# Optimization experiments

Measured on AMD Instinct MI355X. Metric: run time of the kernel, lower is better.

Reference implementation:

```python
import jax, jax.numpy as jnp
import numpy as np

V, D, B, L, A = 50000, 512, 64, 512, 4


def setup_inputs() -> dict:
    key = jax.random.key(0)
    ks = jax.random.split(key, 9)
    emb = jax.random.normal(ks[0], (V, D), jnp.float32) * 0.02
    emb = emb.at[0].set(0.0)  # padding_idx=0 row is zero
    s = 1.0 / np.sqrt(D)
    W_ih = jax.random.uniform(ks[1], (4 * D, 2 * D), jnp.float32, -s, s)
    W_hh = jax.random.uniform(ks[2], (4 * D, D), jnp.float32, -s, s)
    b_ih = jax.random.uniform(ks[3], (4 * D,), jnp.float32, -s, s)
    b_hh = jax.random.uniform(ks[4], (4 * D,), jnp.float32, -s, s)
    X = jax.random.randint(ks[5], (B, L), 0, V, dtype=jnp.int32)
    X_lengths = jax.random.randint(ks[6], (B,), 1, L + 1, dtype=jnp.int32)
    aspect = jax.random.randint(ks[7], (B, A), 0, V, dtype=jnp.int32)
    aspect_lengths = jax.random.randint(ks[8], (B,), 1, A + 1, dtype=jnp.int32)
    return dict(X=X, X_lengths=X_lengths, aspect=aspect, aspect_lengths=aspect_lengths,
                emb=emb, W_ih=W_ih, W_hh=W_hh, b_ih=b_ih, b_hh=b_hh)


def _lstm(embedded, mask, W_ih, W_hh, b_ih, b_hh):
    # embedded: [B, L, 2D], mask: [B, L] bool. Emulates packed LSTM: state only
    # advances on valid steps; padded outputs are zero (pad_packed_sequence).
    Bn = embedded.shape[0]
    Dh = W_hh.shape[1]
    # Precompute input projection for all steps: [L, B, 4D]
    x_proj = (jnp.einsum('blg,hg->blh', embedded, W_ih) + b_ih + b_hh).transpose(1, 0, 2)
    m_seq = mask.T  # [L, B]
    h0 = jnp.zeros((Bn, Dh), embedded.dtype)

    def step(carry, inp):
        h, c = carry
        x_t, m_t = inp
        gates = x_t + h @ W_hh.T  # [B, 4D]
        i, f, g, o = jnp.split(gates, 4, axis=-1)  # PyTorch gate order i,f,g,o
        i = jax.nn.sigmoid(i)
        f = jax.nn.sigmoid(f)
        g = jnp.tanh(g)
        o = jax.nn.sigmoid(o)
        c_new = f * c + i * g
        h_new = o * jnp.tanh(c_new)
        m = m_t[:, None]
        h = jnp.where(m, h_new, h)
        c = jnp.where(m, c_new, c)
        out = jnp.where(m, h_new, jnp.zeros_like(h_new))
        return (h, c), out

    (hT, _), outs = jax.lax.scan(step, (h0, h0), (x_proj, m_seq))
    return outs.transpose(1, 0, 2), hT  # [B, L, D], [B, D]


def reference(X, X_lengths, aspect, aspect_lengths, emb, W_ih, W_hh, b_ih, b_hh):
    word_emb = emb[X]  # [B, L, D]
    # Original uses self.embedding for the aspect ids too (faithful to source).
    asp_emb = emb[aspect].sum(axis=1) / aspect_lengths[:, None].astype(emb.dtype)  # [B, D]
    mask = jnp.arange(word_emb.shape[1])[None, :] < X_lengths[:, None]  # [B, L]
    embedded = jnp.concatenate(
        [word_emb, jnp.broadcast_to(asp_emb[:, None, :], word_emb.shape)], axis=-1)
    embedded = embedded * mask[:, :, None]  # positions >= length stay zero
    output, hT = _lstm(embedded, mask, W_ih, W_hh, b_ih, b_hh)
    hidden = hT[None]  # [1, B, D] like torch (num_layers, B, D)
    return output, hidden, asp_emb
```

## Files before the change

kernel.cpp:

```cpp
#include <hip/hip_runtime.h>


using f32x4  = __attribute__((ext_vector_type(4))) float;
using s16x4  = __attribute__((ext_vector_type(4))) short;
using bf16x8 = __attribute__((ext_vector_type(8))) __bf16;

#define LOG2E 1.4426950408889634f

__device__ __forceinline__ float b2f(short s) {
  union { unsigned u; float f; } c;
  c.u = ((unsigned)(unsigned short)s) << 16;
  return c.f;
}
__device__ __forceinline__ short f2bf(float f) {
  union { float f; unsigned u; } c; c.f = f;
  unsigned r = (c.u + 0x7FFFu + ((c.u >> 16) & 1u)) >> 16;
  return (short)(unsigned short)r;
}
__device__ __forceinline__ float sigm_(float x) {
  float e = __builtin_amdgcn_exp2f(-x * LOG2E);
  return __builtin_amdgcn_rcpf(1.0f + e);
}
__device__ __forceinline__ float tanh_(float x) {
  float e = __builtin_amdgcn_exp2f(x * (2.0f * LOG2E));
  return 1.0f - 2.0f * __builtin_amdgcn_rcpf(1.0f + e);
}

__global__ void k_asp(const int* __restrict__ aspect, const int* __restrict__ alen,
                      const float* __restrict__ emb, float* __restrict__ asp_emb,
                      float* __restrict__ out_asp, unsigned* __restrict__ hbuf) {
  int b = blockIdx.x;
  int t = threadIdx.x;
  {
    unsigned* hz = hbuf + (size_t)(b * 128 + t) * 8;
    #pragma unroll
    for (int i = 0; i < 8; ++i) hz[i] = 0u;
  }
  f32x4 s = {0.f, 0.f, 0.f, 0.f};
  #pragma unroll
  for (int a = 0; a < 4; ++a) {
    int idx = aspect[b * 4 + a];
    s += *(const f32x4*)(emb + (size_t)idx * 512 + t * 4);
  }
  float inv = 1.0f / (float)alen[b];
  s[0] *= inv; s[1] *= inv; s[2] *= inv; s[3] *= inv;
  *(f32x4*)(asp_emb + (size_t)b * 512 + t * 4) = s;
  *(f32x4*)(out_asp + (size_t)b * 512 + t * 4) = s;
}

__global__ void k_pack(const float* __restrict__ W_ih, const float* __restrict__ W_hh,
                       short* __restrict__ W1p, short* __restrict__ Whp) {
  int P = blockIdx.x;
  int t = threadIdx.x;
  int gr = (P & 3) * 512 + (P >> 5) * 8 + ((P >> 2) & 7);
  f32x4 w1 = *(const f32x4*)(W_ih + (size_t)gr * 1024 + t * 4);
  s16x4 o1, oh;
  #pragma unroll
  for (int i = 0; i < 4; ++i) {
    o1[i] = f2bf(w1[i]);
    int c = t * 4 + i;
    int ks = (c & ~7) | (((c & 1) << 2) | ((c >> 1) & 3));
    oh[i] = f2bf(W_hh[(size_t)gr * 512 + ks]);
  }
  *(s16x4*)(W1p + (size_t)P * 512 + t * 4) = o1;
  *(s16x4*)(Whp + (size_t)P * 512 + t * 4) = oh;
}

__global__ void k_aspc(const float* __restrict__ asp_emb, const float* __restrict__ W_ih,
                       const float* __restrict__ b_ih, const float* __restrict__ b_hh,
                       float* __restrict__ aspc) {
  int tid = threadIdx.x;
  int P = blockIdx.x * 32 + (tid >> 3);
  int gr = (P & 3) * 512 + (P >> 5) * 8 + ((P >> 2) & 7);
  const float* wrow = W_ih + (size_t)gr * 1024 + 512;
  float bias = b_ih[gr] + b_hh[gr];
  int b0 = (tid & 7) * 8;
  float a[8];
  #pragma unroll
  for (int i = 0; i < 8; ++i) a[i] = 0.f;
  for (int k = 0; k < 512; k += 4) {
    f32x4 wv = *(const f32x4*)(wrow + k);
    #pragma unroll
    for (int bb = 0; bb < 8; ++bb) {
      f32x4 av = *(const f32x4*)(asp_emb + (size_t)(b0 + bb) * 512 + k);
      a[bb] += wv[0] * av[0] + wv[1] * av[1] + wv[2] * av[2] + wv[3] * av[3];
    }
  }
  #pragma unroll
  for (int bb = 0; bb < 8; ++bb) aspc[(size_t)(b0 + bb) * 2048 + P] = a[bb] + bias;
}

__global__ void k_gather(const int* __restrict__ X, const int* __restrict__ xlen,
                         const float* __restrict__ emb, short* __restrict__ word) {
  int g = blockIdx.x * 256 + threadIdx.x;
  int row = g >> 7;
  int k4 = (g & 127) << 2;
  int b = row >> 9, l = row & 511;
  s16x4 o;
  if (l < xlen[b]) {
    int idx = X[row];
    f32x4 v = *(const f32x4*)(emb + (size_t)idx * 512 + k4);
    o[0] = f2bf(v[0]); o[1] = f2bf(v[1]); o[2] = f2bf(v[2]); o[3] = f2bf(v[3]);
  } else {
    o[0] = 0; o[1] = 0; o[2] = 0; o[3] = 0;
  }
  *(s16x4*)(word + (size_t)row * 512 + k4) = o;
}

__global__ __launch_bounds__(256)
void k_gemm(const short* __restrict__ A, const short* __restrict__ B,
            const float* __restrict__ aspc, const int* __restrict__ xlen,
            short* __restrict__ C) {
  __shared__ char smem[65536];
  const int rt = blockIdx.x, ct = blockIdx.y;
  const int b = rt >> 2;
  if (xlen[b] <= ((rt & 3) << 7)) return;
  const int tid = threadIdx.x;
  const int w = tid >> 6, lane = tid & 63;
  const int lr = lane & 15, lg = lane >> 4;
  const int wr = (w & 1) * 64, wc = (w >> 1) * 64;
  const char* Ab = (const char*)(A + (size_t)rt * 128 * 512);
  const char* Bb = (const char*)(B + (size_t)ct * 128 * 512);

  f32x4 acc[4][4];
  #pragma unroll
  for (int mi = 0; mi < 4; ++mi)
    #pragma unroll
    for (int ni = 0; ni < 4; ++ni) acc[mi][ni] = {0.f, 0.f, 0.f, 0.f};

  auto stage = [&](int kt, int buf) {
    #pragma unroll
    for (int p = 0; p < 4; ++p) {
      int dbase = w * 1024 + p * 4096;
      int d = dbase + (lane << 4);
      int row = d >> 7;
      int kb = (d & 127) ^ (((d >> 9) & 1) << 5);
      __builtin_amdgcn_global_load_lds(
          (const __attribute__((address_space(1))) unsigned*)(Ab + (size_t)row * 1024 + kt * 128 + kb),
          (__attribute__((address_space(3))) unsigned*)(smem + buf * 16384 + dbase), 16, 0, 0);
      __builtin_amdgcn_global_load_lds(
          (const __attribute__((address_space(1))) unsigned*)(Bb + (size_t)row * 1024 + kt * 128 + kb),
          (__attribute__((address_space(3))) unsigned*)(smem + 32768 + buf * 16384 + dbase), 16, 0, 0);
    }
  };

  stage(0, 0);
  __syncthreads();
  #pragma unroll 1
  for (int kt = 0; kt < 8; ++kt) {
    int cur = kt & 1;
    if (kt < 7) stage(kt + 1, cur ^ 1);
    const char* sAc = smem + cur * 16384;
    const char* sBc = smem + 32768 + cur * 16384;
    #pragma unroll
    for (int kk = 0; kk < 2; ++kk) {
      bf16x8 af[4], bfr[4];
      #pragma unroll
      for (int mi = 0; mi < 4; ++mi) {
        int lin = (wr + mi * 16 + lr) * 128 + kk * 64 + lg * 16;
        af[mi] = *(const bf16x8*)(sAc + (lin ^ (((lin >> 9) & 1) << 5)));
      }
      #pragma unroll
      for (int ni = 0; ni < 4; ++ni) {
        int lin = (wc + ni * 16 + lr) * 128 + kk * 64 + lg * 16;
        bfr[ni] = *(const bf16x8*)(sBc + (lin ^ (((lin >> 9) & 1) << 5)));
      }
      #pragma unroll
      for (int mi = 0; mi < 4; ++mi)
        #pragma unroll
        for (int ni = 0; ni < 4; ++ni)
          acc[mi][ni] = __builtin_amdgcn_mfma_f32_16x16x32_bf16(af[mi], bfr[ni], acc[mi][ni], 0, 0, 0);
    }
    __syncthreads();
  }

  const int colb = ct * 128 + wc;
  float cb[4];
  #pragma unroll
  for (int ni = 0; ni < 4; ++ni) cb[ni] = aspc[(size_t)b * 2048 + colb + ni * 16 + lr];
  #pragma unroll
  for (int mi = 0; mi < 4; ++mi) {
    const int row0 = rt * 128 + wr + mi * 16 + lg * 4;
    #pragma unroll
    for (int r = 0; r < 4; ++r) {
      short* crow = C + (size_t)(row0 + r) * 2048 + colb + lr;
      #pragma unroll
      for (int ni = 0; ni < 4; ++ni)
        crow[ni * 16] = f2bf(acc[mi][ni][r] + cb[ni]);
    }
  }
}

__global__ __launch_bounds__(256, 1)
void k_rnn(const short* __restrict__ xproj, const short* __restrict__ Whp,
           const int* __restrict__ xlen, unsigned* hbuf, float* __restrict__ out) {
  __shared__ char wlds[32768];
  const int j = blockIdx.x;
  const int tid = threadIdx.x;
  const int w = tid >> 6;
  const int lane = tid & 63;
  const int lr = lane & 15, lg = lane >> 4;
  const int batch = w * 16 + lr;
  const int mylen = xlen[batch];

  int nt = xlen[batch];
  #pragma unroll
  for (int d = 8; d; d >>= 1) nt = max(nt, __shfl_xor(nt, d));

  {
    const char* src = (const char*)(Whp + (size_t)j * 32 * 512);
    int base = tid * 128;
    int row = base >> 10;
    int c0 = base & 1023;
    #pragma unroll
    for (int i = 0; i < 8; ++i) {
      int c = c0 + i * 16;
      *(f32x4*)(wlds + row * 1024 + (c ^ ((row & 7) << 4))) =
          *(const f32x4*)(src + (size_t)row * 1024 + c);
    }
  }
  __syncthreads();

  float cc0 = 0.f, cc1 = 0.f, h0 = 0.f, h1 = 0.f;
  const short* xbase = xproj + (size_t)batch * 512 * 2048 + j * 32 + lg * 4;
  float* outb = out + (size_t)batch * 512 * 512 + (size_t)j * 8 + lg;
  char* hbB = (char*)hbuf;

  s16x4 xc0 = *(const s16x4*)(xbase);
  s16x4 xc1 = *(const s16x4*)(xbase + 16);
  int i1 = (1 < nt) ? 1 : 0;
  s16x4 xn0 = *(const s16x4*)(xbase + (size_t)i1 * 2048);
  s16x4 xn1 = *(const s16x4*)(xbase + (size_t)i1 * 2048 + 16);

  #pragma unroll 1
  for (int t = 0; t < nt; ++t) {
    f32x4 acc0 = {0.f, 0.f, 0.f, 0.f}, acc1 = {0.f, 0.f, 0.f, 0.f};
    if (t > 0) {
      const char* hb = hbB + (size_t)((t - 1) & 1) * 131072 + batch * 32;
      const unsigned tneed = (unsigned)t;
      int4 qa[16], qb[16];
      unsigned pend = 0xffffu;
      while (pend) {
        #pragma unroll
        for (int kk = 0; kk < 16; ++kk)
          if (pend & (1u << kk)) {
            const char* p = hb + (size_t)(kk * 4 + lg) * 2048;
            asm volatile("global_load_dwordx4 %0, %1, off sc0 sc1"
                         : "=&v"(qa[kk]) : "v"(p) : "memory");
            asm volatile("global_load_dwordx4 %0, %1, off sc0 sc1"
                         : "=&v"(qb[kk]) : "v"(p + 16) : "memory");
          }
        asm volatile("s_waitcnt vmcnt(0)" ::: "memory");
        __builtin_amdgcn_sched_barrier(0);
        #pragma unroll
        for (int kk = 0; kk < 16; ++kk)
          if (pend & (1u << kk)) {
            int4 q0 = qa[kk], q1 = qb[kk];
            unsigned m0 = min((unsigned)q0.x & 0xffffu, (unsigned)q0.y & 0xffffu);
            unsigned m1 = min((unsigned)q0.z & 0xffffu, (unsigned)q0.w & 0xffffu);
            unsigned m2 = min((unsigned)q1.x & 0xffffu, (unsigned)q1.y & 0xffffu);
            unsigned m3 = min((unsigned)q1.z & 0xffffu, (unsigned)q1.w & 0xffffu);
            unsigned mn = min(min(m0, m1), min(m2, m3));
            if (__all(mn >= tneed)) pend &= ~(1u << kk);
          }
      }
      __builtin_amdgcn_sched_barrier(0);
      #pragma unroll
      for (int kk = 0; kk < 16; ++kk) {
        int4 q0 = qa[kk], q1 = qb[kk];
        union { unsigned u[4]; bf16x8 v; } pk;
        pk.u[0] = ((unsigned)q0.x >> 16) | ((unsigned)q0.y & 0xffff0000u);
        pk.u[1] = ((unsigned)q0.z >> 16) | ((unsigned)q0.w & 0xffff0000u);
        pk.u[2] = ((unsigned)q1.x >> 16) | ((unsigned)q1.y & 0xffff0000u);
        pk.u[3] = ((unsigned)q1.z >> 16) | ((unsigned)q1.w & 0xffff0000u);
        int sw = (kk * 64 + lg * 16) ^ ((lr & 7) << 4);
        bf16x8 a0 = *(const bf16x8*)(wlds + lr * 1024 + sw);
        bf16x8 a1 = *(const bf16x8*)(wlds + (16 + lr) * 1024 + sw);
        acc0 = __builtin_amdgcn_mfma_f32_16x16x32_bf16(a0, pk.v, acc0, 0, 0, 0);
        acc1 = __builtin_amdgcn_mfma_f32_16x16x32_bf16(a1, pk.v, acc1, 0, 0, 0);
      }
    }

    const bool m = (t < mylen);
    float hn0, hn1;
    {
      float gi = acc0[0] + b2f(xc0[0]);
      float gf = acc0[1] + b2f(xc0[1]);
      float gg = acc0[2] + b2f(xc0[2]);
      float go = acc0[3] + b2f(xc0[3]);
      float ii = sigm_(gi), ff = sigm_(gf), gv = tanh_(gg), oo = sigm_(go);
      float cn = ff * cc0 + ii * gv;
      hn0 = oo * tanh_(cn);
      cc0 = m ? cn : cc0;
      h0 = m ? hn0 : h0;
    }
    {
      float gi = acc1[0] + b2f(xc1[0]);
      float gf = acc1[1] + b2f(xc1[1]);
      float gg = acc1[2] + b2f(xc1[2]);
      float go = acc1[3] + b2f(xc1[3]);
      float ii = sigm_(gi), ff = sigm_(gf), gv = tanh_(gg), oo = sigm_(go);
      float cn = ff * cc1 + ii * gv;
      hn1 = oo * tanh_(cn);
      cc1 = m ? cn : cc1;
      h1 = m ? hn1 : h1;
    }

    {
      unsigned tag = (unsigned)(t + 1) & 0xffffu;
      unsigned d0 = ((unsigned)(unsigned short)f2bf(h0) << 16) | tag;
      unsigned d1 = ((unsigned)(unsigned short)f2bf(h1) << 16) | tag;
      unsigned long long pr = (unsigned long long)d0 | ((unsigned long long)d1 << 32);
      char* hw = hbB + (size_t)(t & 1) * 131072 + j * 2048 + batch * 32 + lg * 8;
      asm volatile("global_store_dwordx2 %0, %1, off sc0 sc1"
                   :: "v"(hw), "v"(pr) : "memory");
    }

    outb[(size_t)t * 512] = m ? hn0 : 0.0f;
    outb[(size_t)t * 512 + 4] = m ? hn1 : 0.0f;
    int tn = (t + 2 < nt) ? t + 2 : nt - 1;
    const short* xp = xbase + (size_t)tn * 2048;
    xc0 = xn0; xc1 = xn1;
    xn0 = *(const s16x4*)(xp);
    xn1 = *(const s16x4*)(xp + 16);
  }

  for (int t = nt; t < 512; ++t) {
    outb[(size_t)t * 512] = 0.0f;
    outb[(size_t)t * 512 + 4] = 0.0f;
  }

  float* oh = out + (size_t)64 * 512 * 512 + (size_t)batch * 512 + j * 8;
  oh[lg] = h0;
  oh[4 + lg] = h1;
}

extern "C" void kernel_launch(void* const* d_in, const int* in_sizes, int n_in,
                              void* d_out, int out_size, void* d_ws, size_t ws_size,
                              hipStream_t stream) {
  const int*   X      = (const int*)d_in[0];
  const int*   Xlen   = (const int*)d_in[1];
  const int*   aspect = (const int*)d_in[2];
  const int*   alen   = (const int*)d_in[3];
  const float* emb    = (const float*)d_in[4];
  const float* W_ih   = (const float*)d_in[5];
  const float* W_hh   = (const float*)d_in[6];
  const float* b_ih   = (const float*)d_in[7];
  const float* b_hh   = (const float*)d_in[8];
  float* out = (float*)d_out;

  char* ws = (char*)d_ws;
  float*    asp_emb = (float*)(ws + 0);
  float*    aspc    = (float*)(ws + 131072);
  short*    W1p     = (short*)(ws + 655360);
  short*    Whp     = (short*)(ws + 2752512);
  unsigned* hbuf    = (unsigned*)(ws + 4849664);
  short*    word    = (short*)(ws + 5111808);
  short*    xproj   = (short*)(ws + 38666240);

  float* out_hT  = out + (size_t)64 * 512 * 512;
  float* out_asp = out_hT + (size_t)64 * 512;

  hipLaunchKernelGGL(k_asp,    dim3(64),        dim3(128), 0, stream,
                     aspect, alen, emb, asp_emb, out_asp, hbuf);
  hipLaunchKernelGGL(k_pack,   dim3(2048),      dim3(128), 0, stream,
                     W_ih, W_hh, W1p, Whp);
  hipLaunchKernelGGL(k_aspc,   dim3(64),        dim3(256), 0, stream,
                     asp_emb, W_ih, b_ih, b_hh, aspc);
  hipLaunchKernelGGL(k_gather, dim3(16384),     dim3(256), 0, stream,
                     X, Xlen, emb, word);
  hipLaunchKernelGGL(k_gemm,   dim3(256, 16),   dim3(256), 0, stream,
                     word, W1p, aspc, Xlen, xproj);
  hipLaunchKernelGGL(k_rnn,    dim3(64),        dim3(256), 0, stream,
                     xproj, Whp, Xlen, hbuf, out);
}
```

Baseline: 2.100 ms.

## Split LSTM recurrence across 256 blocks grouped per XCC with local/global handoff

The recurrent kernel moves from 64 blocks, each owning hidden units for all batches, to 256 blocks. Each block claims a role through an atomic counter so that the 32 blocks on one XCC share one group of 8 batches. Hidden states are published twice, to a buffer read with XCC-local coherence (sc0) and to a globally coherent copy. Readers poll the local copy first and fall back to the global one, with the aim of cutting cross-die latency in the per-step barrier. The packed W_hh layout and the gate-row permutation change to match, and the risk is role claims failing to land on the expected XCC or stale reads from the non-coherent path.

New measurement: 7.424 ms. 3.54x slower.

```diff
diff --git a/kernel.cpp b/kernel.cpp
--- a/kernel.cpp
+++ b/kernel.cpp
@@ -25,17 +25,23 @@
   float e = __builtin_amdgcn_exp2f(x * (2.0f * LOG2E));
   return 1.0f - 2.0f * __builtin_amdgcn_rcpf(1.0f + e);
 }
+__device__ __forceinline__ void vmcnt0() {
+  asm volatile("s_waitcnt vmcnt(0)" ::: "memory");
+}
 
 __global__ void k_asp(const int* __restrict__ aspect, const int* __restrict__ alen,
                       const float* __restrict__ emb, float* __restrict__ asp_emb,
-                      float* __restrict__ out_asp, unsigned* __restrict__ hbuf) {
+                      float* __restrict__ out_asp, char* __restrict__ zero_mb,
+                      int* __restrict__ role_claim) {
   int b = blockIdx.x;
   int t = threadIdx.x;
   {
-    unsigned* hz = hbuf + (size_t)(b * 128 + t) * 8;
-    #pragma unroll
-    for (int i = 0; i < 8; ++i) hz[i] = 0u;
-  }
+    f32x4 z = {0.f, 0.f, 0.f, 0.f};
+    char* p = zero_mb + (size_t)(b * 128 + t) * 64;
+    *(f32x4*)(p) = z; *(f32x4*)(p + 16) = z;
+    *(f32x4*)(p + 32) = z; *(f32x4*)(p + 48) = z;
+  }
+  if (b >= 62) role_claim[(b - 62) * 128 + t] = 0;
   f32x4 s = {0.f, 0.f, 0.f, 0.f};
   #pragma unroll
   for (int a = 0; a < 4; ++a) {
@@ -52,16 +58,12 @@
                        short* __restrict__ W1p, short* __restrict__ Whp) {
   int P = blockIdx.x;
   int t = threadIdx.x;
-  int gr = (P & 3) * 512 + (P >> 5) * 8 + ((P >> 2) & 7);
+  int gr = (P & 3) * 512 + (P >> 6) * 16 + ((P >> 2) & 15);
   f32x4 w1 = *(const f32x4*)(W_ih + (size_t)gr * 1024 + t * 4);
+  f32x4 wh = *(const f32x4*)(W_hh + (size_t)gr * 512 + t * 4);
   s16x4 o1, oh;
   #pragma unroll
-  for (int i = 0; i < 4; ++i) {
-    o1[i] = f2bf(w1[i]);
-    int c = t * 4 + i;
-    int ks = (c & ~7) | (((c & 1) << 2) | ((c >> 1) & 3));
-    oh[i] = f2bf(W_hh[(size_t)gr * 512 + ks]);
-  }
+  for (int i = 0; i < 4; ++i) { o1[i] = f2bf(w1[i]); oh[i] = f2bf(wh[i]); }
   *(s16x4*)(W1p + (size_t)P * 512 + t * 4) = o1;
   *(s16x4*)(Whp + (size_t)P * 512 + t * 4) = oh;
 }
@@ -71,7 +73,7 @@
                        float* __restrict__ aspc) {
   int tid = threadIdx.x;
   int P = blockIdx.x * 32 + (tid >> 3);
-  int gr = (P & 3) * 512 + (P >> 5) * 8 + ((P >> 2) & 7);
+  int gr = (P & 3) * 512 + (P >> 6) * 16 + ((P >> 2) & 15);
   const float* wrow = W_ih + (size_t)gr * 1024 + 512;
   float bias = b_ih[gr] + b_hh[gr];
   int b0 = (tid & 7) * 8;
@@ -192,65 +194,101 @@
 }
 
 __global__ __launch_bounds__(256, 1)
-void k_rnn(const short* __restrict__ xproj, const short* __restrict__ Whp,
-           const int* __restrict__ xlen, unsigned* hbuf, float* __restrict__ out) {
-  __shared__ char wlds[32768];
-  const int j = blockIdx.x;
+void k_rnn(const short* __restrict__ xproj, const short* __restrict__ Whp2,
+           const int* __restrict__ xlen, char* hpubL, char* hpubG,
+           int* role_claim, float* __restrict__ out) {
+  __shared__ char wlds[65536];
   const int tid = threadIdx.x;
   const int w = tid >> 6;
   const int lane = tid & 63;
-  const int lr = lane & 15, lg = lane >> 4;
-  const int batch = w * 16 + lr;
+  const int lg = lane >> 4, lr = lane & 15;
+
+  if (tid == 0) {
+    unsigned xcc;
+    asm volatile("s_getreg_b32 %0, hwreg(HW_REG_XCC_ID)" : "=s"(xcc));
+    xcc &= 7u;
+    int role = -1;
+    #pragma unroll 1
+    for (int i = 0; i < 32; ++i)
+      if (role < 0 && atomicCAS(&role_claim[(xcc << 5) + i], 0, 1) == 0)
+        role = (xcc << 5) + i;
+    int probe = (xcc << 5) + 31;
+    #pragma unroll 1
+    while (role < 0) {
+      probe = (probe + 1) & 255;
+      if (atomicCAS(&role_claim[probe], 0, 1) == 0) role = probe;
+    }
+    ((volatile int*)wlds)[0] = role;
+  }
+  __syncthreads();
+  const int role = ((volatile int*)wlds)[0];
+  const int g = role >> 5, r = role & 31;
+  __syncthreads();
+
+  {
+    const char* src = (const char*)Whp2 + (size_t)r * 65536;
+    int row = tid >> 2;
+    int c0 = (tid & 3) << 8;
+    #pragma unroll
+    for (int i = 0; i < 16; ++i) {
+      int cbyte = c0 + (i << 4);
+      *(f32x4*)(wlds + row * 1024 + (cbyte ^ ((row & 7) << 4))) =
+          *(const f32x4*)(src + (size_t)row * 1024 + cbyte);
+    }
+  }
+  __syncthreads();
+
+  const int c = lr;
+  const int c7 = c & 7;
+  const bool act = (c < 8);
+  const int batch = (g << 3) + c7;
+  const int uu = (w << 2) + lg;
+  const int uglob = (r << 4) + uu;
   const int mylen = xlen[batch];
-
-  int nt = xlen[batch];
-  #pragma unroll
-  for (int d = 8; d; d >>= 1) nt = max(nt, __shfl_xor(nt, d));
-
-  {
-    const char* src = (const char*)(Whp + (size_t)j * 32 * 512);
-    int base = tid * 128;
-    int row = base >> 10;
-    int c0 = base & 1023;
-    #pragma unroll
-    for (int i = 0; i < 8; ++i) {
-      int c = c0 + i * 16;
-      *(f32x4*)(wlds + row * 1024 + (c ^ ((row & 7) << 4))) =
-          *(const f32x4*)(src + (size_t)row * 1024 + c);
-    }
-  }
-  __syncthreads();
-
-  float cc0 = 0.f, cc1 = 0.f, h0 = 0.f, h1 = 0.f;
-  const short* xbase = xproj + (size_t)batch * 512 * 2048 + j * 32 + lg * 4;
-  float* outb = out + (size_t)batch * 512 * 512 + (size_t)j * 8 + lg;
-  char* hbB = (char*)hbuf;
-
-  s16x4 xc0 = *(const s16x4*)(xbase);
-  s16x4 xc1 = *(const s16x4*)(xbase + 16);
-  int i1 = (1 < nt) ? 1 : 0;
-  s16x4 xn0 = *(const s16x4*)(xbase + (size_t)i1 * 2048);
-  s16x4 xn1 = *(const s16x4*)(xbase + (size_t)i1 * 2048 + 16);
+  int nt = xlen[(g << 3) + (lane & 7)];
+  #pragma unroll
+  for (int d = 4; d; d >>= 1) nt = max(nt, __shfl_xor(nt, d));
+
+  const short* xbase = xproj + (size_t)batch * 1048576 + (r << 6) + (w << 4) + (lg << 2);
+  float* outb = out + (size_t)batch * 262144 + uglob;
+
+  float cc = 0.f, hh = 0.f;
+  s16x4 xc = *(const s16x4*)(xbase);
 
   #pragma unroll 1
   for (int t = 0; t < nt; ++t) {
-    f32x4 acc0 = {0.f, 0.f, 0.f, 0.f}, acc1 = {0.f, 0.f, 0.f, 0.f};
+    f32x4 acc = {0.f, 0.f, 0.f, 0.f};
     if (t > 0) {
-      const char* hb = hbB + (size_t)((t - 1) & 1) * 131072 + batch * 32;
       const unsigned tneed = (unsigned)t;
+      const size_t mboff = (size_t)(((((t - 1) & 1) << 3) + g) * 16384) + (size_t)c7 * 2048;
+      const char* mbL = hpubL + mboff;
+      const char* mbG = hpubG + mboff;
       int4 qa[16], qb[16];
       unsigned pend = 0xffffu;
+      int pass = 0;
       while (pend) {
-        #pragma unroll
-        for (int kk = 0; kk < 16; ++kk)
-          if (pend & (1u << kk)) {
-            const char* p = hb + (size_t)(kk * 4 + lg) * 2048;
-            asm volatile("global_load_dwordx4 %0, %1, off sc0 sc1"
-                         : "=&v"(qa[kk]) : "v"(p) : "memory");
-            asm volatile("global_load_dwordx4 %0, %1, off sc0 sc1"
-                         : "=&v"(qb[kk]) : "v"(p + 16) : "memory");
-          }
-        asm volatile("s_waitcnt vmcnt(0)" ::: "memory");
+        if (pass < 3) {
+          #pragma unroll
+          for (int kk = 0; kk < 16; ++kk)
+            if (pend & (1u << kk)) {
+              const char* p = mbL + (kk << 7) + (lg << 5);
+              asm volatile("global_load_dwordx4 %0, %1, off sc0"
+                           : "=&v"(qa[kk]) : "v"(p) : "memory");
+              asm volatile("global_load_dwordx4 %0, %1, off sc0"
+                           : "=&v"(qb[kk]) : "v"(p + 16) : "memory");
+            }
+        } else {
+          #pragma unroll
+          for (int kk = 0; kk < 16; ++kk)
+            if (pend & (1u << kk)) {
+              const char* p = mbG + (kk << 7) + (lg << 5);
+              asm volatile("global_load_dwordx4 %0, %1, off sc0 sc1"
+                           : "=&v"(qa[kk]) : "v"(p) : "memory");
+              asm volatile("global_load_dwordx4 %0, %1, off sc0 sc1"
+                           : "=&v"(qb[kk]) : "v"(p + 16) : "memory");
+            }
+        }
+        vmcnt0();
         __builtin_amdgcn_sched_barrier(0);
         #pragma unroll
         for (int kk = 0; kk < 16; ++kk)
@@ -263,8 +301,10 @@
             unsigned mn = min(min(m0, m1), min(m2, m3));
             if (__all(mn >= tneed)) pend &= ~(1u << kk);
           }
+        ++pass;
       }
       __builtin_amdgcn_sched_barrier(0);
+      const char* wrow = wlds + (size_t)(w * 16 + lr) * 1024;
       #pragma unroll
       for (int kk = 0; kk < 16; ++kk) {
         int4 q0 = qa[kk], q1 = qb[kk];
@@ -273,66 +313,43 @@
         pk.u[1] = ((unsigned)q0.z >> 16) | ((unsigned)q0.w & 0xffff0000u);
         pk.u[2] = ((unsigned)q1.x >> 16) | ((unsigned)q1.y & 0xffff0000u);
         pk.u[3] = ((unsigned)q1.z >> 16) | ((unsigned)q1.w & 0xffff0000u);
-        int sw = (kk * 64 + lg * 16) ^ ((lr & 7) << 4);
-        bf16x8 a0 = *(const bf16x8*)(wlds + lr * 1024 + sw);
-        bf16x8 a1 = *(const bf16x8*)(wlds + (16 + lr) * 1024 + sw);
-        acc0 = __builtin_amdgcn_mfma_f32_16x16x32_bf16(a0, pk.v, acc0, 0, 0, 0);
-        acc1 = __builtin_amdgcn_mfma_f32_16x16x32_bf16(a1, pk.v, acc1, 0, 0, 0);
+        int swo = ((kk << 6) + (lg << 4)) ^ ((lr & 7) << 4);
+        bf16x8 a = *(const bf16x8*)(wrow + swo);
+        acc = __builtin_amdgcn_mfma_f32_16x16x32_bf16(a, pk.v, acc, 0, 0, 0);
       }
     }
 
-    const bool m = (t < mylen);
-    float hn0, hn1;
-    {
-      float gi = acc0[0] + b2f(xc0[0]);
-      float gf = acc0[1] + b2f(xc0[1]);
-      float gg = acc0[2] + b2f(xc0[2]);
-      float go = acc0[3] + b2f(xc0[3]);
-      float ii = sigm_(gi), ff = sigm_(gf), gv = tanh_(gg), oo = sigm_(go);
-      float cn = ff * cc0 + ii * gv;
-      hn0 = oo * tanh_(cn);
-      cc0 = m ? cn : cc0;
-      h0 = m ? hn0 : h0;
-    }
-    {
-      float gi = acc1[0] + b2f(xc1[0]);
-      float gf = acc1[1] + b2f(xc1[1]);
-      float gg = acc1[2] + b2f(xc1[2]);
-      float go = acc1[3] + b2f(xc1[3]);
-      float ii = sigm_(gi), ff = sigm_(gf), gv = tanh_(gg), oo = sigm_(go);
-      float cn = ff * cc1 + ii * gv;
-      hn1 = oo * tanh_(cn);
-      cc1 = m ? cn : cc1;
-      h1 = m ? hn1 : h1;
-    }
-
-    {
-      unsigned tag = (unsigned)(t + 1) & 0xffffu;
-      unsigned d0 = ((unsigned)(unsigned short)f2bf(h0) << 16) | tag;
-      unsigned d1 = ((unsigned)(unsigned short)f2bf(h1) << 16) | tag;
-      unsigned long long pr = (unsigned long long)d0 | ((unsigned long long)d1 << 32);
-      char* hw = hbB + (size_t)(t & 1) * 131072 + j * 2048 + batch * 32 + lg * 8;
-      asm volatile("global_store_dwordx2 %0, %1, off sc0 sc1"
-                   :: "v"(hw), "v"(pr) : "memory");
-    }
-
-    outb[(size_t)t * 512] = m ? hn0 : 0.0f;
-    outb[(size_t)t * 512 + 4] = m ? hn1 : 0.0f;
-    int tn = (t + 2 < nt) ? t + 2 : nt - 1;
-    const short* xp = xbase + (size_t)tn * 2048;
-    xc0 = xn0; xc1 = xn1;
-    xn0 = *(const s16x4*)(xp);
-    xn1 = *(const s16x4*)(xp + 16);
-  }
-
-  for (int t = nt; t < 512; ++t) {
-    outb[(size_t)t * 512] = 0.0f;
-    outb[(size_t)t * 512 + 4] = 0.0f;
-  }
-
-  float* oh = out + (size_t)64 * 512 * 512 + (size_t)batch * 512 + j * 8;
-  oh[lg] = h0;
-  oh[4 + lg] = h1;
+    const bool m = act && (t < mylen);
+    float gi = acc[0] + b2f(xc[0]);
+    float gf = acc[1] + b2f(xc[1]);
+    float gg = acc[2] + b2f(xc[2]);
+    float go = acc[3] + b2f(xc[3]);
+    float ii = sigm_(gi), ff = sigm_(gf), gv = tanh_(gg), oo = sigm_(go);
+    float cn = ff * cc + ii * gv;
+    float hn = oo * tanh_(cn);
+    cc = m ? cn : cc;
+    hh = m ? hn : hh;
+
+    if (act) {
+      unsigned dwv = ((unsigned)(unsigned short)f2bf(hh) << 16)
+                   | ((unsigned)(t + 1) & 0xffffu);
+      size_t po = (size_t)((((t & 1) << 3) + g) * 16384) + (size_t)c * 2048
+                + (size_t)uglob * 4;
+      char* pL = hpubL + po;
+      char* pG = hpubG + po;
+      asm volatile("global_store_dword %0, %1, off sc0" :: "v"(pL), "v"(dwv) : "memory");
+      asm volatile("global_store_dword %0, %1, off sc0 sc1" :: "v"(pG), "v"(dwv) : "memory");
+      outb[(size_t)t * 512] = m ? hn : 0.0f;
+    }
+    int tn = (t + 1 < nt) ? t + 1 : t;
+    xc = *(const s16x4*)(xbase + (size_t)tn * 2048);
+  }
+
+  if (act) {
+    #pragma unroll 1
+    for (int t = nt; t < 512; ++t) outb[(size_t)t * 512] = 0.0f;
+    out[(1u << 24) + (size_t)batch * 512 + uglob] = hh;
+  }
 }
 
 extern "C" void kernel_launch(void* const* d_in, const int* in_sizes, int n_in,
@@ -350,27 +367,29 @@
   float* out = (float*)d_out;
 
   char* ws = (char*)d_ws;
-  float*    asp_emb = (float*)(ws + 0);
-  float*    aspc    = (float*)(ws + 131072);
-  short*    W1p     = (short*)(ws + 655360);
-  short*    Whp     = (short*)(ws + 2752512);
-  unsigned* hbuf    = (unsigned*)(ws + 4849664);
-  short*    word    = (short*)(ws + 5111808);
-  short*    xproj   = (short*)(ws + 38666240);
+  float* asp_emb    = (float*)(ws + 0);
+  float* aspc       = (float*)(ws + 131072);
+  short* W1p        = (short*)(ws + 655360);
+  short* Whp2       = (short*)(ws + 2752512);
+  char*  hpubL      = (char*)(ws + 4849664);
+  char*  hpubG      = (char*)(ws + 5111808);
+  int*   role_claim = (int*)(ws + 5373952);
+  short* word       = (short*)(ws + 5378048);
+  short* xproj      = (short*)(ws + 38932480);
 
   float* out_hT  = out + (size_t)64 * 512 * 512;
   float* out_asp = out_hT + (size_t)64 * 512;
 
   hipLaunchKernelGGL(k_asp,    dim3(64),        dim3(128), 0, stream,
-                     aspect, alen, emb, asp_emb, out_asp, hbuf);
+                     aspect, alen, emb, asp_emb, out_asp, hpubL, role_claim);
   hipLaunchKernelGGL(k_pack,   dim3(2048),      dim3(128), 0, stream,
-                     W_ih, W_hh, W1p, Whp);
+                     W_ih, W_hh, W1p, Whp2);
   hipLaunchKernelGGL(k_aspc,   dim3(64),        dim3(256), 0, stream,
                      asp_emb, W_ih, b_ih, b_hh, aspc);
   hipLaunchKernelGGL(k_gather, dim3(16384),     dim3(256), 0, stream,
                      X, Xlen, emb, word);
   hipLaunchKernelGGL(k_gemm,   dim3(256, 16),   dim3(256), 0, stream,
                      word, W1p, aspc, Xlen, xproj);
-  hipLaunchKernelGGL(k_rnn,    dim3(64),        dim3(256), 0, stream,
-                     xproj, Whp, Xlen, hbuf, out);
-}
+  hipLaunchKernelGGL(k_rnn,    dim3(256),       dim3(256), 0, stream,
+                     xproj, Whp2, Xlen, hpubL, hpubG, role_claim, out);
+}
```
